# Kernel optimization log

Measured on AMD Instinct MI355X. Metric: run time of the kernel, lower is better.

Reference implementation:

```python
import jax, jax.numpy as jnp
import numpy as np

N = 100000   # nodes
E = 1600000  # edges


def setup_inputs() -> dict:
    key = jax.random.key(0)
    ks = jax.random.split(key, 9)
    return {
        "in_feat": jax.random.normal(ks[0], (N, 256), jnp.float32),
        "W": jax.random.normal(ks[1], (256, 128), jnp.float32) * 0.05,
        "attn_l": jax.random.normal(ks[2], (1, 128), jnp.float32) * 0.1,
        "attn_r": jax.random.normal(ks[3], (1, 128), jnp.float32) * 0.1,
        "bias": jax.random.normal(ks[4], (1, 128), jnp.float32) * 0.01,
        "fc_w": jax.random.normal(ks[5], (128, 2), jnp.float32) * 0.1,
        "fc_b": jax.random.normal(ks[6], (2,), jnp.float32) * 0.01,
        "src": jax.random.randint(ks[7], (E,), 0, N, jnp.int32),
        "dst": jax.random.randint(ks[8], (E,), 0, N, jnp.int32),
    }


def reference(in_feat, W, attn_l, attn_r, bias, fc_w, fc_b, src, dst):
    # GATConv, num_heads=1 (head dim kept implicit since it is squeezed anyway)
    h = in_feat @ W                              # [N, F] projected features
    el = jnp.sum(h * attn_l, axis=-1)            # [N] left attention logits
    er = jnp.sum(h * attn_r, axis=-1)            # [N] right attention logits
    e = jax.nn.leaky_relu(el[src] + er[dst], negative_slope=0.2)  # [E]
    # edge softmax segmented by destination node (numerically stable)
    m = jax.ops.segment_max(e, dst, num_segments=N)               # [N]
    ex = jnp.exp(e - m[dst])                                      # [E]
    s = jax.ops.segment_sum(ex, dst, num_segments=N)              # [N]
    alpha = ex / jnp.where(s == 0, 1.0, s)[dst]                   # [E]
    # attention-weighted aggregation of source features to destinations
    agg = jax.ops.segment_sum(alpha[:, None] * h[src], dst, num_segments=N)  # [N, F]
    agg = agg + bias                                              # GATConv bias
    # head: ReLU -> Linear -> sigmoid
    out = jax.nn.sigmoid(jax.nn.relu(agg) @ fc_w + fc_b)          # [N, C]
    return out
```

## Files before the change

kernel.cpp:

```cpp
#include <hip/hip_runtime.h>
#include <cstdint>
#include <cstddef>

#define N_NODES 100000
#define E_EDGES 1600000
#define F_IN 256
#define F_OUT 128
#define NBKT 391
#define OBCAP 5120

typedef __attribute__((ext_vector_type(8))) short  short8v;
typedef __attribute__((ext_vector_type(4))) float  float4v;

__device__ __forceinline__ unsigned short f2bf(float x) {
    union { float f; unsigned u; } v; v.f = x;
    unsigned r = v.u + 0x7fffu + ((v.u >> 16) & 1u);
    return (unsigned short)(r >> 16);
}

__global__ __launch_bounds__(256) void wcvt_kernel(const float* __restrict__ W,
                                                   unsigned short* __restrict__ Wt) {
    int t = blockIdx.x * 256 + threadIdx.x;
    if (t >= F_IN * F_OUT) return;
    int k = t >> 7, j = t & 127;
    Wt[j * F_IN + k] = f2bf(W[t]);
}

__global__ __launch_bounds__(256) void gemm_mfma(const float* __restrict__ A,
                                                 const unsigned short* __restrict__ Wt,
                                                 const float* __restrict__ attn_l,
                                                 const float* __restrict__ attn_r,
                                                 unsigned short* __restrict__ Hb,
                                                 float* __restrict__ el,
                                                 float* __restrict__ er) {
    __shared__ unsigned short As[64 * 64];
    __shared__ unsigned short Bs[128 * 64];
    int tid  = threadIdx.x;
    int wave = tid >> 6, lane = tid & 63;
    int g = lane >> 4, c = lane & 15;
    int row0 = blockIdx.x * 64;
    float4v acc[8] = {};

    for (int k0 = 0; k0 < F_IN; k0 += 64) {
        {
            int r  = tid >> 2;
            int ks = (tid & 3) * 16;
            int grow = row0 + r;
            unsigned short tmp[16];
            if (grow < N_NODES) {
                const float* ap = A + (size_t)grow * F_IN + k0 + ks;
                #pragma unroll
                for (int i = 0; i < 4; ++i) {
                    float4 v = reinterpret_cast<const float4*>(ap)[i];
                    tmp[i*4+0] = f2bf(v.x); tmp[i*4+1] = f2bf(v.y);
                    tmp[i*4+2] = f2bf(v.z); tmp[i*4+3] = f2bf(v.w);
                }
            } else {
                #pragma unroll
                for (int i = 0; i < 16; ++i) tmp[i] = 0;
            }
            int u0 = (r * 64 + ks) ^ ((r & 7) << 3);
            int u1 = (r * 64 + ks + 8) ^ ((r & 7) << 3);
            *reinterpret_cast<short8v*>(&As[u0]) = *reinterpret_cast<short8v*>(&tmp[0]);
            *reinterpret_cast<short8v*>(&As[u1]) = *reinterpret_cast<short8v*>(&tmp[8]);
        }
        {
            int j   = tid >> 1;
            int ks2 = (tid & 1) * 32;
            const short8v* wp = reinterpret_cast<const short8v*>(Wt + (size_t)j * F_IN + k0 + ks2);
            #pragma unroll
            for (int i = 0; i < 4; ++i) {
                int u = (j * 64 + ks2 + 8 * i) ^ ((j & 7) << 3);
                *reinterpret_cast<short8v*>(&Bs[u]) = wp[i];
            }
        }
        __syncthreads();
        #pragma unroll
        for (int ks = 0; ks < 2; ++ks) {
            int arow = wave * 16 + c;
            int aoff = (arow * 64 + ks * 32 + g * 8) ^ ((arow & 7) << 3);
            short8v af = *reinterpret_cast<short8v*>(&As[aoff]);
            #pragma unroll
            for (int nt = 0; nt < 8; ++nt) {
                int j = nt * 16 + c;
                int boff = (j * 64 + ks * 32 + g * 8) ^ ((j & 7) << 3);
                short8v bf = *reinterpret_cast<short8v*>(&Bs[boff]);
                acc[nt] = __builtin_amdgcn_mfma_f32_16x16x32_bf16(af, bf, acc[nt], 0, 0, 0);
            }
        }
        __syncthreads();
    }

    float al[8], ar[8];
    #pragma unroll
    for (int nt = 0; nt < 8; ++nt) {
        al[nt] = attn_l[nt * 16 + c];
        ar[nt] = attn_r[nt * 16 + c];
    }
    #pragma unroll
    for (int r = 0; r < 4; ++r) {
        int grow = row0 + wave * 16 + g * 4 + r;
        float sl = 0.f, sr = 0.f;
        #pragma unroll
        for (int nt = 0; nt < 8; ++nt) {
            float h = acc[nt][r];
            sl += h * al[nt];
            sr += h * ar[nt];
        }
        if (grow < N_NODES) {
            #pragma unroll
            for (int nt = 0; nt < 8; ++nt)
                Hb[(size_t)grow * F_OUT + nt * 16 + c] = f2bf(acc[nt][r]);
        }
        #pragma unroll
        for (int off = 1; off < 16; off <<= 1) {
            sl += __shfl_xor(sl, off);
            sr += __shfl_xor(sr, off);
        }
        if (c == 0 && grow < N_NODES) { el[grow] = sl; er[grow] = sr; }
    }
}

__global__ __launch_bounds__(256) void k_hist1(const int* __restrict__ dst,
                                               int* __restrict__ bcnt) {
    __shared__ int h[NBKT];
    int t = threadIdx.x;
    for (int i = t; i < NBKT; i += 256) h[i] = 0;
    __syncthreads();
    int e0  = blockIdx.x * 4096;
    int end = min(e0 + 4096, E_EDGES);
    for (int i = e0 + t; i < end; i += 256) atomicAdd(&h[dst[i] >> 8], 1);
    __syncthreads();
    for (int i = t; i < NBKT; i += 256) if (h[i]) atomicAdd(&bcnt[i], h[i]);
}

__global__ __launch_bounds__(512) void k_scan(const int* __restrict__ bcnt,
                                              int* __restrict__ bbase,
                                              int* __restrict__ bcur) {
    __shared__ int s[512];
    int t = threadIdx.x;
    int d = (t < NBKT) ? bcnt[t] : 0;
    s[t] = d;
    __syncthreads();
    for (int off = 1; off < 512; off <<= 1) {
        int v = (t >= off) ? s[t - off] : 0;
        __syncthreads();
        s[t] += v;
        __syncthreads();
    }
    if (t < NBKT) { int ex = s[t] - d; bbase[t] = ex; bcur[t] = ex; }
    if (t == NBKT - 1) bbase[NBKT] = s[t];
}

__global__ __launch_bounds__(256) void k_scatter1(const int* __restrict__ src,
                                                  const int* __restrict__ dst,
                                                  int* __restrict__ bcur,
                                                  unsigned int* __restrict__ epack) {
    __shared__ int h[NBKT];
    int t = threadIdx.x;
    for (int i = t; i < NBKT; i += 256) h[i] = 0;
    __syncthreads();
    int e0  = blockIdx.x * 4096;
    int end = min(e0 + 4096, E_EDGES);
    #pragma unroll
    for (int j = 0; j < 16; ++j) {
        int i = e0 + j * 256 + t;
        if (i < end) atomicAdd(&h[dst[i] >> 8], 1);
    }
    __syncthreads();
    for (int i = t; i < NBKT; i += 256) {
        int c = h[i];
        h[i] = c ? atomicAdd(&bcur[i], c) : 0;
    }
    __syncthreads();
    #pragma unroll
    for (int j = 0; j < 16; ++j) {
        int i = e0 + j * 256 + t;
        if (i < end) {
            int dv = dst[i];
            int p = atomicAdd(&h[dv >> 8], 1);
            epack[p] = (unsigned)src[i] | ((unsigned)(dv & 255) << 17);
        }
    }
}

__global__ __launch_bounds__(256) void k_sort2(const unsigned int* __restrict__ epack,
                                               const int* __restrict__ bbase,
                                               int* __restrict__ esrc,
                                               int* __restrict__ rowptr,
                                               int* __restrict__ deg) {
    __shared__ int hist[256], cur[256], s[256];
    __shared__ int obuf[OBCAP];
    int b = blockIdx.x, t = threadIdx.x;
    int base = bbase[b], end = bbase[b + 1];
    int cnt  = end - base;
    hist[t] = 0;
    __syncthreads();
    for (int i = t; i < cnt; i += 256) atomicAdd(&hist[epack[base + i] >> 17], 1);
    __syncthreads();
    int d = hist[t];
    s[t] = d;
    __syncthreads();
    for (int off = 1; off < 256; off <<= 1) {
        int v = (t >= off) ? s[t - off] : 0;
        __syncthreads();
        s[t] += v;
        __syncthreads();
    }
    int excl = s[t] - d;
    int n = b * 256 + t;
    if (n < N_NODES) { deg[n] = d; rowptr[n] = base + excl; }
    cur[t] = excl;
    __syncthreads();
    for (int i = t; i < cnt; i += 256) {
        unsigned e = epack[base + i];
        int p = atomicAdd(&cur[e >> 17], 1);
        if (p < OBCAP) obuf[p] = (int)(e & 0x1FFFFu);
    }
    __syncthreads();
    for (int i = t; i < cnt; i += 256) esrc[base + i] = obuf[i];
}

__global__ __launch_bounds__(256) void agg_fused(const int* __restrict__ rowptr,
                                                 const int* __restrict__ deg,
                                                 const int* __restrict__ esrc,
                                                 const float* __restrict__ el,
                                                 const float* __restrict__ er,
                                                 const unsigned int* __restrict__ H2,
                                                 const float* __restrict__ bias,
                                                 const float* __restrict__ fcw,
                                                 const float* __restrict__ fcb,
                                                 float* __restrict__ out) {
    __shared__ float2 exbuf[4][64];
    int tid   = threadIdx.x;
    int wslot = tid >> 6;
    int wid   = (blockIdx.x * 256 + tid) >> 6;
    int lane  = tid & 63;
    if (wid >= N_NODES) return;
    int start = rowptr[wid];
    int dg    = deg[wid];
    float ern = er[wid];
    float m = -3.4e38f, ssum = 0.f;
    float2 acc = make_float2(0.f, 0.f);
    float2* eb = exbuf[wslot];

    for (int base = 0; base < dg; base += 64) {
        int cnt = min(64, dg - base);
        int sid = 0;
        float x = -3.4e38f;
        if (lane < cnt) {
            sid = esrc[start + base + lane];
            float tv = el[sid] + ern;
            x = tv > 0.f ? tv : 0.2f * tv;
        }
        float cm = x;
        #pragma unroll
        for (int off = 32; off; off >>= 1) cm = fmaxf(cm, __shfl_xor(cm, off));
        float mn = fmaxf(m, cm);
        float r  = __expf(m - mn);
        float ex = (lane < cnt) ? __expf(x - mn) : 0.f;
        float cs = ex;
        #pragma unroll
        for (int off = 32; off; off >>= 1) cs += __shfl_xor(cs, off);
        ssum = ssum * r + cs;
        acc.x *= r; acc.y *= r;
        m = mn;
        eb[lane] = make_float2(ex, __int_as_float(sid));
        __builtin_amdgcn_wave_barrier();
        int q = 0;
        for (; q + 4 <= cnt; q += 4) {
            float2 p0 = eb[q+0], p1 = eb[q+1], p2 = eb[q+2], p3 = eb[q+3];
            unsigned v0 = H2[(size_t)__float_as_int(p0.y) * 64 + lane];
            unsigned v1 = H2[(size_t)__float_as_int(p1.y) * 64 + lane];
            unsigned v2 = H2[(size_t)__float_as_int(p2.y) * 64 + lane];
            unsigned v3 = H2[(size_t)__float_as_int(p3.y) * 64 + lane];
            acc.x += p0.x * __uint_as_float(v0 << 16);
            acc.y += p0.x * __uint_as_float(v0 & 0xffff0000u);
            acc.x += p1.x * __uint_as_float(v1 << 16);
            acc.y += p1.x * __uint_as_float(v1 & 0xffff0000u);
            acc.x += p2.x * __uint_as_float(v2 << 16);
            acc.y += p2.x * __uint_as_float(v2 & 0xffff0000u);
            acc.x += p3.x * __uint_as_float(v3 << 16);
            acc.y += p3.x * __uint_as_float(v3 & 0xffff0000u);
        }
        for (; q < cnt; ++q) {
            float2 p0 = eb[q];
            unsigned v0 = H2[(size_t)__float_as_int(p0.y) * 64 + lane];
            acc.x += p0.x * __uint_as_float(v0 << 16);
            acc.y += p0.x * __uint_as_float(v0 & 0xffff0000u);
        }
        __builtin_amdgcn_wave_barrier();
    }

    float scale = ssum > 0.f ? 1.f / ssum : 0.f;
    float2 bv = ((const float2*)bias)[lane];
    float v0 = fmaxf(acc.x * scale + bv.x, 0.f);
    float v1 = fmaxf(acc.y * scale + bv.y, 0.f);
    float4 wv = ((const float4*)fcw)[lane];
    float d0 = v0 * wv.x + v1 * wv.z;
    float d1 = v0 * wv.y + v1 * wv.w;
    #pragma unroll
    for (int off = 32; off; off >>= 1) {
        d0 += __shfl_down(d0, off);
        d1 += __shfl_down(d1, off);
    }
    if (lane == 0) {
        out[(size_t)wid * 2 + 0] = 1.f / (1.f + __expf(-(d0 + fcb[0])));
        out[(size_t)wid * 2 + 1] = 1.f / (1.f + __expf(-(d1 + fcb[1])));
    }
}

extern "C" void kernel_launch(void* const* d_in, const int* in_sizes, int n_in,
                              void* d_out, int out_size, void* d_ws, size_t ws_size,
                              hipStream_t stream) {
    const float* in_feat = (const float*)d_in[0];
    const float* W       = (const float*)d_in[1];
    const float* attn_l  = (const float*)d_in[2];
    const float* attn_r  = (const float*)d_in[3];
    const float* bias    = (const float*)d_in[4];
    const float* fc_w    = (const float*)d_in[5];
    const float* fc_b    = (const float*)d_in[6];
    const int*   src     = (const int*)d_in[7];
    const int*   dst     = (const int*)d_in[8];
    float* out = (float*)d_out;

    char* p = (char*)d_ws;
    unsigned short* HB = (unsigned short*)p; p += (size_t)N_NODES * F_OUT * sizeof(unsigned short);
    unsigned short* WT = (unsigned short*)p; p += (size_t)F_IN * F_OUT * sizeof(unsigned short);
    float* EL     = (float*)p; p += (size_t)N_NODES * sizeof(float);
    float* ER     = (float*)p; p += (size_t)N_NODES * sizeof(float);
    int*   DEG    = (int*)p;   p += (size_t)N_NODES * sizeof(int);
    int*   ROWPTR = (int*)p;   p += (size_t)N_NODES * sizeof(int);
    int*   BCNT   = (int*)p;   p += 512 * sizeof(int);
    int*   BBASE  = (int*)p;   p += 512 * sizeof(int);
    int*   BCUR   = (int*)p;   p += 512 * sizeof(int);
    unsigned int* EPACK = (unsigned int*)p; p += (size_t)E_EDGES * sizeof(unsigned int);
    int*   ESRC   = (int*)p;   p += (size_t)E_EDGES * sizeof(int);

    hipMemsetAsync(BCNT, 0, 512 * sizeof(int), stream);

    wcvt_kernel<<<(F_IN * F_OUT + 255) / 256, 256, 0, stream>>>(W, WT);
    gemm_mfma<<<(N_NODES + 63) / 64, 256, 0, stream>>>(in_feat, WT, attn_l, attn_r, HB, EL, ER);

    k_hist1   <<<NBKT, 256, 0, stream>>>(dst, BCNT);
    k_scan    <<<1, 512, 0, stream>>>(BCNT, BBASE, BCUR);
    k_scatter1<<<NBKT, 256, 0, stream>>>(src, dst, BCUR, EPACK);
    k_sort2   <<<NBKT, 256, 0, stream>>>(EPACK, BBASE, ESRC, ROWPTR, DEG);

    agg_fused<<<(N_NODES * 64 + 255) / 256, 256, 0, stream>>>(
        ROWPTR, DEG, ESRC, EL, ER, (const unsigned int*)HB, bias, fc_w, fc_b, out);
}
```

Measured before the change: 159.7 us.

## Use direct global-to-LDS loads in GEMM and byte-offset gathers in aggregation

The GEMM now stages fp32 A tiles and bf16 W tiles into LDS with global_load_lds, which bypasses registers, and uses a new swizzle. The bf16 conversion moves to the LDS read side through v_cvt_pk_bf16_f32. The aggregation kernel precomputes 32-bit byte offsets per source row so each gather needs less 64-bit address arithmetic. In exchange the A tile in LDS doubles in size, out-of-range rows are clamped rather than zeroed, and 32-bit offsets assume H stays under 4GB.

```diff
diff --git a/kernel.cpp b/kernel.cpp
--- a/kernel.cpp
+++ b/kernel.cpp
@@ -9,6 +9,9 @@
 #define NBKT 391
 #define OBCAP 5120
 
+#define GLOBAL_AS __attribute__((address_space(1)))
+#define LDS_AS    __attribute__((address_space(3)))
+
 typedef __attribute__((ext_vector_type(8))) short  short8v;
 typedef __attribute__((ext_vector_type(4))) float  float4v;
 
@@ -16,6 +19,12 @@
     union { float f; unsigned u; } v; v.f = x;
     unsigned r = v.u + 0x7fffu + ((v.u >> 16) & 1u);
     return (unsigned short)(r >> 16);
+}
+
+__device__ __forceinline__ unsigned cvt_pk_bf16(float lo, float hi) {
+    unsigned r;
+    asm("v_cvt_pk_bf16_f32 %0, %1, %2" : "=v"(r) : "v"(lo), "v"(hi));
+    return r;
 }
 
 __global__ __launch_bounds__(256) void wcvt_kernel(const float* __restrict__ W,
@@ -33,7 +42,7 @@
                                                  unsigned short* __restrict__ Hb,
                                                  float* __restrict__ el,
                                                  float* __restrict__ er) {
-    __shared__ unsigned short As[64 * 64];
+    __shared__ float          Afs[64 * 64];
     __shared__ unsigned short Bs[128 * 64];
     int tid  = threadIdx.x;
     int wave = tid >> 6, lane = tid & 63;
@@ -41,45 +50,52 @@
     int row0 = blockIdx.x * 64;
     float4v acc[8] = {};
 
+    int a_r[4], a_k[4], a_w[4];
+    #pragma unroll
+    for (int i = 0; i < 4; ++i) {
+        int W_ = i * 1024 + tid * 4;
+        int r  = W_ >> 6;
+        a_w[i] = W_;
+        a_r[i] = min(row0 + r, N_NODES - 1);
+        a_k[i] = (W_ & 63) ^ ((r & 15) << 2);
+    }
+    int b_j[4], b_k[4], b_u[4];
+    #pragma unroll
+    for (int i = 0; i < 4; ++i) {
+        int U_ = i * 2048 + tid * 8;
+        int j  = U_ >> 6;
+        b_u[i] = U_;
+        b_j[i] = j;
+        b_k[i] = (U_ & 63) ^ ((j & 7) << 3);
+    }
+
     for (int k0 = 0; k0 < F_IN; k0 += 64) {
-        {
-            int r  = tid >> 2;
-            int ks = (tid & 3) * 16;
-            int grow = row0 + r;
-            unsigned short tmp[16];
-            if (grow < N_NODES) {
-                const float* ap = A + (size_t)grow * F_IN + k0 + ks;
-                #pragma unroll
-                for (int i = 0; i < 4; ++i) {
-                    float4 v = reinterpret_cast<const float4*>(ap)[i];
-                    tmp[i*4+0] = f2bf(v.x); tmp[i*4+1] = f2bf(v.y);
-                    tmp[i*4+2] = f2bf(v.z); tmp[i*4+3] = f2bf(v.w);
-                }
-            } else {
-                #pragma unroll
-                for (int i = 0; i < 16; ++i) tmp[i] = 0;
-            }
-            int u0 = (r * 64 + ks) ^ ((r & 7) << 3);
-            int u1 = (r * 64 + ks + 8) ^ ((r & 7) << 3);
-            *reinterpret_cast<short8v*>(&As[u0]) = *reinterpret_cast<short8v*>(&tmp[0]);
-            *reinterpret_cast<short8v*>(&As[u1]) = *reinterpret_cast<short8v*>(&tmp[8]);
-        }
-        {
-            int j   = tid >> 1;
-            int ks2 = (tid & 1) * 32;
-            const short8v* wp = reinterpret_cast<const short8v*>(Wt + (size_t)j * F_IN + k0 + ks2);
-            #pragma unroll
-            for (int i = 0; i < 4; ++i) {
-                int u = (j * 64 + ks2 + 8 * i) ^ ((j & 7) << 3);
-                *reinterpret_cast<short8v*>(&Bs[u]) = wp[i];
-            }
-        }
-        __syncthreads();
+        #pragma unroll
+        for (int i = 0; i < 4; ++i) {
+            __builtin_amdgcn_global_load_lds(
+                (const GLOBAL_AS unsigned int*)(A + (size_t)a_r[i] * F_IN + k0 + a_k[i]),
+                (LDS_AS unsigned int*)&Afs[a_w[i]], 16, 0, 0);
+        }
+        #pragma unroll
+        for (int i = 0; i < 4; ++i) {
+            __builtin_amdgcn_global_load_lds(
+                (const GLOBAL_AS unsigned int*)(Wt + (size_t)b_j[i] * F_IN + k0 + b_k[i]),
+                (LDS_AS unsigned int*)&Bs[b_u[i]], 16, 0, 0);
+        }
+        __syncthreads();
+        int arow = wave * 16 + c;
+        int aswz = (arow & 15) << 2;
         #pragma unroll
         for (int ks = 0; ks < 2; ++ks) {
-            int arow = wave * 16 + c;
-            int aoff = (arow * 64 + ks * 32 + g * 8) ^ ((arow & 7) << 3);
-            short8v af = *reinterpret_cast<short8v*>(&As[aoff]);
+            int woff = arow * 64 + ks * 32 + g * 8;
+            float4 a0 = *reinterpret_cast<float4*>(&Afs[(woff)     ^ aswz]);
+            float4 a1 = *reinterpret_cast<float4*>(&Afs[(woff + 4) ^ aswz]);
+            unsigned u[4];
+            u[0] = cvt_pk_bf16(a0.x, a0.y);
+            u[1] = cvt_pk_bf16(a0.z, a0.w);
+            u[2] = cvt_pk_bf16(a1.x, a1.y);
+            u[3] = cvt_pk_bf16(a1.z, a1.w);
+            short8v af = *reinterpret_cast<short8v*>(u);
             #pragma unroll
             for (int nt = 0; nt < 8; ++nt) {
                 int j = nt * 16 + c;
@@ -226,7 +242,7 @@
                                                  const int* __restrict__ esrc,
                                                  const float* __restrict__ el,
                                                  const float* __restrict__ er,
-                                                 const unsigned int* __restrict__ H2,
+                                                 const char* __restrict__ Hc,
                                                  const float* __restrict__ bias,
                                                  const float* __restrict__ fcw,
                                                  const float* __restrict__ fcb,
@@ -243,15 +259,17 @@
     float m = -3.4e38f, ssum = 0.f;
     float2 acc = make_float2(0.f, 0.f);
     float2* eb = exbuf[wslot];
+    unsigned lane4 = (unsigned)lane << 2;
 
     for (int base = 0; base < dg; base += 64) {
         int cnt = min(64, dg - base);
-        int sid = 0;
+        unsigned rowb = 0;
         float x = -3.4e38f;
         if (lane < cnt) {
-            sid = esrc[start + base + lane];
-            float tv = el[sid] + ern;
+            int sid = esrc[start + base + lane];
+            float tv = el[(unsigned)sid] + ern;
             x = tv > 0.f ? tv : 0.2f * tv;
+            rowb = (unsigned)sid << 8;
         }
         float cm = x;
         #pragma unroll
@@ -265,15 +283,15 @@
         ssum = ssum * r + cs;
         acc.x *= r; acc.y *= r;
         m = mn;
-        eb[lane] = make_float2(ex, __int_as_float(sid));
+        eb[lane] = make_float2(ex, __uint_as_float(rowb));
         __builtin_amdgcn_wave_barrier();
         int q = 0;
         for (; q + 4 <= cnt; q += 4) {
             float2 p0 = eb[q+0], p1 = eb[q+1], p2 = eb[q+2], p3 = eb[q+3];
-            unsigned v0 = H2[(size_t)__float_as_int(p0.y) * 64 + lane];
-            unsigned v1 = H2[(size_t)__float_as_int(p1.y) * 64 + lane];
-            unsigned v2 = H2[(size_t)__float_as_int(p2.y) * 64 + lane];
-            unsigned v3 = H2[(size_t)__float_as_int(p3.y) * 64 + lane];
+            unsigned v0 = *(const unsigned*)(Hc + (__float_as_uint(p0.y) + lane4));
+            unsigned v1 = *(const unsigned*)(Hc + (__float_as_uint(p1.y) + lane4));
+            unsigned v2 = *(const unsigned*)(Hc + (__float_as_uint(p2.y) + lane4));
+            unsigned v3 = *(const unsigned*)(Hc + (__float_as_uint(p3.y) + lane4));
             acc.x += p0.x * __uint_as_float(v0 << 16);
             acc.y += p0.x * __uint_as_float(v0 & 0xffff0000u);
             acc.x += p1.x * __uint_as_float(v1 << 16);
@@ -285,7 +303,7 @@
         }
         for (; q < cnt; ++q) {
             float2 p0 = eb[q];
-            unsigned v0 = H2[(size_t)__float_as_int(p0.y) * 64 + lane];
+            unsigned v0 = *(const unsigned*)(Hc + (__float_as_uint(p0.y) + lane4));
             acc.x += p0.x * __uint_as_float(v0 << 16);
             acc.y += p0.x * __uint_as_float(v0 & 0xffff0000u);
         }
@@ -348,5 +366,5 @@
     k_sort2   <<<NBKT, 256, 0, stream>>>(EPACK, BBASE, ESRC, ROWPTR, DEG);
 
     agg_fused<<<(N_NODES * 64 + 255) / 256, 256, 0, stream>>>(
-        ROWPTR, DEG, ESRC, EL, ER, (const unsigned int*)HB, bias, fc_w, fc_b, out);
-}
+        ROWPTR, DEG, ESRC, EL, ER, (const char*)HB, bias, fc_w, fc_b, out);
+}
```

Result: no change. 157.2 us (-1.6%).
